# Optimization experiments

Hardware: AMD Instinct MI355X
Metric: run time of the kernel (lower is better)

Reference implementation:

```python
import jax, jax.numpy as jnp
import numpy as np


def setup_inputs() -> dict:
    key = jax.random.key(0)
    ks = jax.random.split(key, 4)
    B, C, H, W = 4, 512, 64, 64
    A = 512  # attention_dim
    x = jax.random.normal(ks[0], (B, C, H, W), dtype=jnp.float32)
    # 1x1 conv weights as [out_ch, in_ch] matrices (kaiming-like scale)
    scale = np.sqrt(2.0 / C).astype(np.float32)
    Wq = jax.random.normal(ks[1], (A, C), dtype=jnp.float32) * scale
    Wk = jax.random.normal(ks[2], (A, C), dtype=jnp.float32) * scale
    Wv = jax.random.normal(ks[3], (C, C), dtype=jnp.float32) * scale
    bq = jnp.zeros((A,), dtype=jnp.float32)
    bk = jnp.zeros((A,), dtype=jnp.float32)
    bv = jnp.zeros((C,), dtype=jnp.float32)
    return {"x": x, "Wq": Wq, "bq": bq, "Wk": Wk, "bk": bk, "Wv": Wv, "bv": bv}


def reference(x, Wq, bq, Wk, bk, Wv, bv):
    B, C, H, W = x.shape
    N = H * W
    xf = x.reshape(B, C, N)  # [B, C, N]
    # 1x1 convs == per-pixel channel matmuls
    q = jnp.einsum('ac,bcn->bna', Wq, xf) + bq[None, None, :]   # [B, N, A] (query, permuted)
    k = jnp.einsum('ac,bcn->ban', Wk, xf) + bk[None, :, None]   # [B, A, N] (key)
    v = jnp.einsum('oc,bcn->bno', Wv, xf) + bv[None, None, :]   # [B, N, C] (value, permuted)
    attn = jnp.einsum('bna,bam->bnm', q, k)                     # [B, N, N]
    attn = jax.nn.softmax(attn, axis=-2)                        # softmax over dim=-2 (queries)
    out = jnp.einsum('bnm,bmc->bnc', attn, v)                   # [B, N, C]
    # Faithful to torch: .view(B, C, H, W) reinterprets the [B, N, C] buffer
    out = out.reshape(B, C, H, W)
    return x + 0.1 * out
```

## Files before the change

kernel.cpp:

```cpp
#include <hip/hip_runtime.h>
#include <stdint.h>


#define LDT 40
#define SUB 5120

typedef _Float16 f16x8 __attribute__((ext_vector_type(8)));
typedef float f32x4 __attribute__((ext_vector_type(4)));

__device__ __forceinline__ void async16(const _Float16* g, _Float16* l)
{
  __builtin_amdgcn_global_load_lds(
      (const __attribute__((address_space(1))) void*)g,
      (__attribute__((address_space(3))) void*)l, 16, 0, 0);
}

#define WAIT_VM8() asm volatile("s_waitcnt vmcnt(8)" ::: "memory")
#define WAIT_VM0() asm volatile("s_waitcnt vmcnt(0)" ::: "memory")

template <int ASRC, int EPI, int NSUB, int STG>
__global__ void __launch_bounds__(256, 2) gemm_f16(
    const _Float16* __restrict__ Ap, long lda, long zsa,
    const _Float16* __restrict__ Bp, long ldb, long zsb,
    int kslice,
    const _Float16* __restrict__ fs16, long zsl,
    float* __restrict__ outF, _Float16* __restrict__ outH, long ldc, long zso,
    const float* __restrict__ bias0, const float* __restrict__ bias1,
    const float* __restrict__ xadd,
    float* __restrict__ pmax, float* __restrict__ psum, long zsp,
    float alpha)
{
  constexpr int SMEM_E = (STG == 1) ? (4 * NSUB * 4096) : (2 * NSUB * SUB);
  __shared__ _Float16 smem[SMEM_E];

  const int z = blockIdx.z;
  const long i0 = (long)blockIdx.x * 128;
  const long j0 = (long)blockIdx.y * 128;
  const int t = (int)threadIdx.x;
  const int lane = t & 63;
  const int wv = t >> 6;
  const int quad = lane >> 4;
  const int lrow = lane & 15;
  const int wm = (wv & 1) << 6;
  const int wn = (wv >> 1) << 6;

  f32x4 acc[4][4];
  const f32x4 fz = {0.f, 0.f, 0.f, 0.f};
#pragma unroll
  for (int a = 0; a < 4; a++)
#pragma unroll
    for (int b = 0; b < 4; b++) acc[a][b] = fz;

  if constexpr (STG == 0) {
    const int r0 = t >> 2;
    const int s0 = (t & 3) << 3;

    const _Float16* gA0 = Ap + z * zsa + (i0 + r0) * lda + s0;
    const _Float16* gA1 = gA0 + 64 * lda;
    const _Float16* gB0 = Bp + z * zsb + (j0 + r0) * ldb + s0;
    const _Float16* gB1 = gB0 + 64 * ldb;
    const int la0 = r0 * LDT + s0;
    const int la1 = (r0 + 64) * LDT + s0;

    for (int kk = 0; kk < kslice; kk += 32 * NSUB) {
      f16x8 va[NSUB][2], vb[NSUB][2];
#pragma unroll
      for (int s = 0; s < NSUB; s++) {
        va[s][0] = *(const f16x8*)(gA0 + kk + 32 * s);
        va[s][1] = *(const f16x8*)(gA1 + kk + 32 * s);
        vb[s][0] = *(const f16x8*)(gB0 + kk + 32 * s);
        vb[s][1] = *(const f16x8*)(gB1 + kk + 32 * s);
      }
      __syncthreads();
#pragma unroll
      for (int s = 0; s < NSUB; s++) {
        *(f16x8*)&smem[s * SUB + la0] = va[s][0];
        *(f16x8*)&smem[s * SUB + la1] = va[s][1];
        *(f16x8*)&smem[(NSUB + s) * SUB + la0] = vb[s][0];
        *(f16x8*)&smem[(NSUB + s) * SUB + la1] = vb[s][1];
      }
      __syncthreads();

#pragma unroll
      for (int h = 0; h < NSUB; h++) {
        const _Float16* pA = smem + h * SUB;
        const _Float16* pB = smem + (NSUB + h) * SUB;
        f16x8 fa[4], fb[4];
#pragma unroll
        for (int f = 0; f < 4; f++) {
          fa[f] = *(const f16x8*)&pA[(wm + f * 16 + lrow) * LDT + quad * 8];
          fb[f] = *(const f16x8*)&pB[(wn + f * 16 + lrow) * LDT + quad * 8];
        }
#pragma unroll
        for (int fm = 0; fm < 4; fm++)
#pragma unroll
          for (int fn = 0; fn < 4; fn++)
            acc[fm][fn] = __builtin_amdgcn_mfma_f32_16x16x32_f16(fa[fm], fb[fn], acc[fm][fn], 0, 0, 0);
      }
    }
  } else {
    constexpr int KSTEP = 32 * NSUB;
    constexpr int BUFE = 2 * NSUB * 4096;
    const int crow = lane >> 2;
    const int ks8 = (((lane & 3) ^ ((lane >> 3) & 3)) << 3);

    const _Float16* gAc0 = Ap + z * zsa + (i0 + 16 * wv + crow) * lda + ks8;
    const _Float16* gAc1 = gAc0 + 64 * lda;
    const _Float16* gBc0 = Bp + z * zsb + (j0 + 16 * wv + crow) * ldb + ks8;
    const _Float16* gBc1 = gBc0 + 64 * ldb;
    _Float16* ldsC0 = smem + wv * 512;
    _Float16* ldsC1 = smem + (wv + 4) * 512;

    const _Float16* fsZq = nullptr;
    if constexpr (ASRC == 1)
      fsZq = fs16 + z * zsl + (long)blockIdx.x * 4096 + quad * 8;

    const int qs = ((quad ^ ((lrow >> 1) & 3)) << 3);

    auto stage = [&](int buf, int kk) {
#pragma unroll
      for (int s = 0; s < NSUB; s++) {
        const int ab = buf * BUFE + s * 4096;
        const int bb = buf * BUFE + (NSUB + s) * 4096;
        async16(gAc0 + kk + 32 * s, ldsC0 + ab);
        async16(gAc1 + kk + 32 * s, ldsC1 + ab);
        async16(gBc0 + kk + 32 * s, ldsC0 + bb);
        async16(gBc1 + kk + 32 * s, ldsC1 + bb);
      }
    };

    stage(0, 0);
    int cur = 0;
    for (int kk = 0; kk < kslice; kk += KSTEP) {
      f16x8 fsv[NSUB];
      if constexpr (ASRC == 1) {
#pragma unroll
        for (int h = 0; h < NSUB; h++)
          fsv[h] = *(const f16x8*)(fsZq + kk + 32 * h);
      }
      if (kk + KSTEP < kslice) {
        stage(cur ^ 1, kk + KSTEP);
        WAIT_VM8();
      } else {
        WAIT_VM0();
      }
      __builtin_amdgcn_s_barrier();

#pragma unroll
      for (int h = 0; h < NSUB; h++) {
        const _Float16* pA = smem + cur * BUFE + h * 4096;
        const _Float16* pB = smem + cur * BUFE + (NSUB + h) * 4096;
        f16x8 fa[4], fb[4];
#pragma unroll
        for (int f = 0; f < 4; f++) {
          fa[f] = *(const f16x8*)&pA[(wm + f * 16 + lrow) * 32 + qs];
          fb[f] = *(const f16x8*)&pB[(wn + f * 16 + lrow) * 32 + qs];
        }
        if constexpr (ASRC == 1) {
#pragma unroll
          for (int f = 0; f < 4; f++) fa[f] = fa[f] * fsv[h];
        }
#pragma unroll
        for (int fm = 0; fm < 4; fm++)
#pragma unroll
          for (int fn = 0; fn < 4; fn++)
            acc[fm][fn] = __builtin_amdgcn_mfma_f32_16x16x32_f16(fa[fm], fb[fn], acc[fm][fn], 0, 0, 0);
      }
      __builtin_amdgcn_s_barrier();
      cur ^= 1;
    }
  }

  const long obase = (long)z * zso;

  if constexpr (EPI == 1 || EPI == 2) {
#pragma unroll
    for (int fm = 0; fm < 4; fm++) {
      const long gi0 = i0 + wm + fm * 16 + quad * 4;
#pragma unroll
      for (int fn = 0; fn < 4; fn++) {
        const long gj = j0 + wn + fn * 16 + lrow;
        float badd = 0.f;
        if constexpr (EPI == 1) badd = (gj < 512) ? bias0[gj] : bias1[gj - 512];
#pragma unroll
        for (int r = 0; r < 4; r++) {
          float v = acc[fm][fn][r];
          if constexpr (EPI == 1) v += badd;
          else v += bias0[gi0 + r];
          outH[obase + (gi0 + r) * ldc + gj] = (_Float16)v;
        }
      }
    }
  } else if constexpr (EPI == 3) {
#pragma unroll
    for (int fm = 0; fm < 4; fm++) {
      const long gi0 = i0 + wm + fm * 16 + quad * 4;
#pragma unroll
      for (int fn = 0; fn < 4; fn++) {
        const long gj = j0 + wn + fn * 16 + lrow;
#pragma unroll
        for (int r = 0; r < 4; r++) {
          const long o = obase + (gi0 + r) * ldc + gj;
          outF[o] = fmaf(alpha, acc[fm][fn][r], xadd[o]);
        }
      }
    }
  } else {
    __syncthreads();
    float* Ls = (float*)smem;
#pragma unroll
    for (int fn = 0; fn < 4; fn++) {
      float mx = -3.4e38f;
#pragma unroll
      for (int fm = 0; fm < 4; fm++)
#pragma unroll
        for (int r = 0; r < 4; r++) mx = fmaxf(mx, acc[fm][fn][r]);
      Ls[(wv * 4 + quad) * 64 + fn * 16 + lrow] = mx;
    }
    __syncthreads();
    {
      const int c = t & 127;
      const int h = t >> 7;
      const int wvv = ((c >> 6) << 1) + h;
      const int wc = c & 63;
      float M = -3.4e38f;
#pragma unroll
      for (int q = 0; q < 4; q++) M = fmaxf(M, Ls[(wvv * 4 + q) * 64 + wc]);
      Ls[1024 + h * 128 + c] = M;
    }
    __syncthreads();
    if (t < 128) {
      float Mcol = fmaxf(Ls[1024 + t], Ls[1152 + t]);
      pmax[z * zsp + (long)blockIdx.x * 4096 + j0 + t] = Mcol;
      Ls[1280 + t] = Mcol;
    }
    __syncthreads();
#pragma unroll
    for (int fn = 0; fn < 4; fn++) {
      const int colc = wn + fn * 16 + lrow;
      const float Mcol = Ls[1280 + colc];
      const long gj = j0 + colc;
      float sm = 0.f;
#pragma unroll
      for (int fm = 0; fm < 4; fm++) {
        const long gi0 = i0 + wm + fm * 16 + quad * 4;
#pragma unroll
        for (int r = 0; r < 4; r++) {
          float e = __expf(acc[fm][fn][r] - Mcol);
          sm += e;
          outH[obase + (gi0 + r) * ldc + gj] = (_Float16)e;
        }
      }
      Ls[(wv * 4 + quad) * 64 + fn * 16 + lrow] = sm;
    }
    __syncthreads();
    if (t < 128) {
      const int wc = t & 63;
      const int ch = t >> 6;
      float s = 0.f;
#pragma unroll
      for (int h = 0; h < 2; h++) {
        const int wvv = (ch << 1) + h;
#pragma unroll
        for (int q = 0; q < 4; q++) s += Ls[(wvv * 4 + q) * 64 + wc];
      }
      psum[z * zsp + (long)blockIdx.x * 4096 + j0 + t] = s;
    }
  }
}

__global__ void convert_weights(const float* __restrict__ Wq, const float* __restrict__ Wk,
                                const float* __restrict__ Wv,
                                _Float16* __restrict__ WQK, _Float16* __restrict__ Wv16)
{
  int idx = blockIdx.x * 256 + threadIdx.x;
  if (idx < 524288)
    WQK[idx] = (_Float16)((idx < 262144) ? Wq[idx] : Wk[idx - 262144]);
  else
    Wv16[idx - 524288] = (_Float16)Wv[idx - 524288];
}

__global__ void transpose_x(const float* __restrict__ x, _Float16* __restrict__ xT)
{
  __shared__ float tile[32][33];
  const int b = blockIdx.z;
  const int n0 = blockIdx.x * 32;
  const int c0 = blockIdx.y * 32;
  const int tx = threadIdx.x;
  const int ty = threadIdx.y;
  const float* xb = x + (long)b * 2097152;
#pragma unroll
  for (int k = 0; k < 4; k++)
    tile[ty + k * 8][tx] = xb[(long)(c0 + ty + k * 8) * 4096 + n0 + tx];
  __syncthreads();
  _Float16* xTb = xT + (long)b * 2097152;
#pragma unroll
  for (int k = 0; k < 4; k++)
    xTb[(long)(n0 + ty + k * 8) * 512 + c0 + tx] = (_Float16)tile[tx][ty + k * 8];
}

__global__ void stats_scale(const float* __restrict__ pmax, const float* __restrict__ psum,
                            _Float16* __restrict__ fs16)
{
  const int idx = blockIdx.x * 256 + threadIdx.x;
  const int z = idx >> 12;
  const int m = idx & 4095;
  const float* pm = pmax + (long)z * 131072 + m;
  const float* ps = psum + (long)z * 131072 + m;
  float M = -3.4e38f, S = 0.f;
  for (int i = 0; i < 32; i++) {
    float m2 = pm[(long)i * 4096], s2 = ps[(long)i * 4096];
    float nm = fmaxf(M, m2);
    S = S * __expf(M - nm) + s2 * __expf(m2 - nm);
    M = nm;
  }
  const float lse = M + __logf(S);
  _Float16* fo = fs16 + (long)z * 131072 + m;
  for (int i = 0; i < 32; i++)
    fo[(long)i * 4096] = (_Float16)__expf(pm[(long)i * 4096] - lse);
}

extern "C" void kernel_launch(void* const* d_in, const int* in_sizes, int n_in,
                              void* d_out, int out_size, void* d_ws, size_t ws_size,
                              hipStream_t stream)
{
  const float* x  = (const float*)d_in[0];
  const float* Wq = (const float*)d_in[1];
  const float* bq = (const float*)d_in[2];
  const float* Wk = (const float*)d_in[3];
  const float* bk = (const float*)d_in[4];
  const float* Wv = (const float*)d_in[5];
  const float* bv = (const float*)d_in[6];
  float* out = (float*)d_out;

  char* w = (char*)d_ws;
  _Float16* WQK   = (_Float16*)(w + 0);
  _Float16* Wv16  = (_Float16*)(w + 1048576);
  _Float16* xT    = (_Float16*)(w + 1572864);
  _Float16* QK    = (_Float16*)(w + 18350080);
  _Float16* Vt    = (_Float16*)(w + 51904512);
  float*    pmaxB = (float*)   (w + 68747264);
  float*    psumB = (float*)   (w + 70844416);
  _Float16* fs16  = (_Float16*)(w + 72941568);
  _Float16* S16   = (_Float16*)(w + 75038720);

  convert_weights<<<3072, 256, 0, stream>>>(Wq, Wk, Wv, WQK, Wv16);
  transpose_x<<<dim3(128, 16, 4), dim3(32, 8), 0, stream>>>(x, xT);

  gemm_f16<0, 1, 2, 0><<<dim3(32, 8, 4), 256, 0, stream>>>(
      xT, 512, 2097152L, WQK, 512, 0L, 512, nullptr, 0L,
      nullptr, QK, 1024, 4194304L, bq, bk, nullptr, nullptr, nullptr, 0L, 0.f);
  gemm_f16<0, 2, 2, 0><<<dim3(4, 32, 4), 256, 0, stream>>>(
      Wv16, 512, 0L, xT, 512, 2097152L, 512, nullptr, 0L,
      nullptr, Vt, 4096, 2097152L, bv, nullptr, nullptr, nullptr, nullptr, 0L, 0.f);
  gemm_f16<0, 4, 2, 1><<<dim3(32, 32, 4), 256, 0, stream>>>(
      QK, 1024, 4194304L, QK + 512, 1024, 4194304L, 512, nullptr, 0L,
      nullptr, S16, 4096, 16777216L, nullptr, nullptr, nullptr,
      pmaxB, psumB, 131072L, 0.f);
  stats_scale<<<64, 256, 0, stream>>>(pmaxB, psumB, fs16);
  gemm_f16<1, 3, 2, 1><<<dim3(32, 4, 4), 256, 0, stream>>>(
      S16, 4096, 16777216L, Vt, 4096, 2097152L, 4096, fs16, 131072L,
      out, nullptr, 512, 2097152L, nullptr, nullptr, x, nullptr, nullptr, 0L, 0.1f);
}
```

Before: 310.9 us.

## Restructure async GEMM pipeline into per-32-K ring buffers with tunable occupancy

The STG=1 GEMM path now stages one 32-wide K slice per buffer. The S·Q^T GEMM uses a double buffer with half the LDS, and launch bounds allow 4 blocks per CU. The attn·V GEMM uses a 4-deep ring that keeps 3 slices in flight. The per-column softmax scale vector is preloaded into LDS once instead of being read from global memory every iteration. This aims to raise occupancy and hide global-load latency, at the cost of more barriers per K unit and tighter register limits at occupancy 4.

```diff
diff --git a/kernel.cpp b/kernel.cpp
--- a/kernel.cpp
+++ b/kernel.cpp
@@ -15,11 +15,10 @@
       (__attribute__((address_space(3))) void*)l, 16, 0, 0);
 }
 
-#define WAIT_VM8() asm volatile("s_waitcnt vmcnt(8)" ::: "memory")
-#define WAIT_VM0() asm volatile("s_waitcnt vmcnt(0)" ::: "memory")
-
-template <int ASRC, int EPI, int NSUB, int STG>
-__global__ void __launch_bounds__(256, 2) gemm_f16(
+#define WVM(N) asm volatile("s_waitcnt vmcnt(" #N ")" ::: "memory")
+
+template <int ASRC, int EPI, int NSUB, int STG, int OCC>
+__global__ void __launch_bounds__(256, OCC) gemm_f16(
     const _Float16* __restrict__ Ap, long lda, long zsa,
     const _Float16* __restrict__ Bp, long ldb, long zsb,
     int kslice,
@@ -30,7 +29,8 @@
     float* __restrict__ pmax, float* __restrict__ psum, long zsp,
     float alpha)
 {
-  constexpr int SMEM_E = (STG == 1) ? (4 * NSUB * 4096) : (2 * NSUB * SUB);
+  constexpr int SMEM_E = (STG == 1) ? (NSUB * 8192 + (ASRC == 1 ? 4096 : 0))
+                                    : (2 * NSUB * SUB);
   __shared__ _Float16 smem[SMEM_E];
 
   const int z = blockIdx.z;
@@ -99,8 +99,6 @@
       }
     }
   } else {
-    constexpr int KSTEP = 32 * NSUB;
-    constexpr int BUFE = 2 * NSUB * 4096;
     const int crow = lane >> 2;
     const int ks8 = (((lane & 3) ^ ((lane >> 3) & 3)) << 3);
 
@@ -108,66 +106,65 @@
     const _Float16* gAc1 = gAc0 + 64 * lda;
     const _Float16* gBc0 = Bp + z * zsb + (j0 + 16 * wv + crow) * ldb + ks8;
     const _Float16* gBc1 = gBc0 + 64 * ldb;
-    _Float16* ldsC0 = smem + wv * 512;
-    _Float16* ldsC1 = smem + (wv + 4) * 512;
-
-    const _Float16* fsZq = nullptr;
+
+    const int qs = ((quad ^ ((lrow >> 1) & 3)) << 3);
+
+    auto stage = [&](int buf, int kk2) {
+      _Float16* base = smem + buf * 8192;
+      async16(gAc0 + kk2, base + wv * 512);
+      async16(gAc1 + kk2, base + 2048 + wv * 512);
+      async16(gBc0 + kk2, base + 4096 + wv * 512);
+      async16(gBc1 + kk2, base + 6144 + wv * 512);
+    };
+
+    _Float16* fsL = nullptr;
+    if constexpr (ASRC == 1) {
+      fsL = smem + NSUB * 8192;
+      const _Float16* fsrc = fs16 + z * zsl + (long)blockIdx.x * 4096;
+      *(f16x8*)&fsL[t * 16] = *(const f16x8*)&fsrc[t * 16];
+      *(f16x8*)&fsL[t * 16 + 8] = *(const f16x8*)&fsrc[t * 16 + 8];
+    }
+    stage(0, 0);
+    if constexpr (NSUB == 4) { stage(1, 32); stage(2, 64); }
     if constexpr (ASRC == 1)
-      fsZq = fs16 + z * zsl + (long)blockIdx.x * 4096 + quad * 8;
-
-    const int qs = ((quad ^ ((lrow >> 1) & 3)) << 3);
-
-    auto stage = [&](int buf, int kk) {
-#pragma unroll
-      for (int s = 0; s < NSUB; s++) {
-        const int ab = buf * BUFE + s * 4096;
-        const int bb = buf * BUFE + (NSUB + s) * 4096;
-        async16(gAc0 + kk + 32 * s, ldsC0 + ab);
-        async16(gAc1 + kk + 32 * s, ldsC1 + ab);
-        async16(gBc0 + kk + 32 * s, ldsC0 + bb);
-        async16(gBc1 + kk + 32 * s, ldsC1 + bb);
-      }
-    };
-
-    stage(0, 0);
-    int cur = 0;
-    for (int kk = 0; kk < kslice; kk += KSTEP) {
-      f16x8 fsv[NSUB];
+      asm volatile("s_waitcnt lgkmcnt(0)" ::: "memory");
+    __builtin_amdgcn_s_barrier();
+
+    int ib = 0;
+    for (int kk = 0; kk < kslice; kk += 32, ++ib) {
+      const int rem = kslice - kk;
+      if constexpr (NSUB == 4) {
+        if (rem > 96) { stage((ib + 3) & 3, kk + 96); WVM(12); }
+        else if (rem > 64) { WVM(8); }
+        else if (rem > 32) { WVM(4); }
+        else { WVM(0); }
+      } else {
+        if (rem > 32) { stage((ib + 1) & 1, kk + 32); WVM(4); }
+        else { WVM(0); }
+      }
+      __builtin_amdgcn_s_barrier();
+
+      const int cur = ib & (NSUB - 1);
+      const _Float16* pA = smem + cur * 8192;
+      const _Float16* pB = pA + 4096;
+      f16x8 fa[4], fb[4];
+#pragma unroll
+      for (int f = 0; f < 4; f++) {
+        fa[f] = *(const f16x8*)&pA[(wm + f * 16 + lrow) * 32 + qs];
+        fb[f] = *(const f16x8*)&pB[(wn + f * 16 + lrow) * 32 + qs];
+      }
       if constexpr (ASRC == 1) {
-#pragma unroll
-        for (int h = 0; h < NSUB; h++)
-          fsv[h] = *(const f16x8*)(fsZq + kk + 32 * h);
-      }
-      if (kk + KSTEP < kslice) {
-        stage(cur ^ 1, kk + KSTEP);
-        WAIT_VM8();
-      } else {
-        WAIT_VM0();
-      }
+        const f16x8 fsv = *(const f16x8*)&fsL[kk + quad * 8];
+#pragma unroll
+        for (int f = 0; f < 4; f++) fa[f] = fa[f] * fsv;
+      }
+#pragma unroll
+      for (int fm = 0; fm < 4; fm++)
+#pragma unroll
+        for (int fn = 0; fn < 4; fn++)
+          acc[fm][fn] = __builtin_amdgcn_mfma_f32_16x16x32_f16(fa[fm], fb[fn], acc[fm][fn], 0, 0, 0);
+
       __builtin_amdgcn_s_barrier();
-
-#pragma unroll
-      for (int h = 0; h < NSUB; h++) {
-        const _Float16* pA = smem + cur * BUFE + h * 4096;
-        const _Float16* pB = smem + cur * BUFE + (NSUB + h) * 4096;
-        f16x8 fa[4], fb[4];
-#pragma unroll
-        for (int f = 0; f < 4; f++) {
-          fa[f] = *(const f16x8*)&pA[(wm + f * 16 + lrow) * 32 + qs];
-          fb[f] = *(const f16x8*)&pB[(wn + f * 16 + lrow) * 32 + qs];
-        }
-        if constexpr (ASRC == 1) {
-#pragma unroll
-          for (int f = 0; f < 4; f++) fa[f] = fa[f] * fsv[h];
-        }
-#pragma unroll
-        for (int fm = 0; fm < 4; fm++)
-#pragma unroll
-          for (int fn = 0; fn < 4; fn++)
-            acc[fm][fn] = __builtin_amdgcn_mfma_f32_16x16x32_f16(fa[fm], fb[fn], acc[fm][fn], 0, 0, 0);
-      }
-      __builtin_amdgcn_s_barrier();
-      cur ^= 1;
     }
   }
 
@@ -347,18 +344,18 @@
   convert_weights<<<3072, 256, 0, stream>>>(Wq, Wk, Wv, WQK, Wv16);
   transpose_x<<<dim3(128, 16, 4), dim3(32, 8), 0, stream>>>(x, xT);
 
-  gemm_f16<0, 1, 2, 0><<<dim3(32, 8, 4), 256, 0, stream>>>(
+  gemm_f16<0, 1, 2, 0, 2><<<dim3(32, 8, 4), 256, 0, stream>>>(
       xT, 512, 2097152L, WQK, 512, 0L, 512, nullptr, 0L,
       nullptr, QK, 1024, 4194304L, bq, bk, nullptr, nullptr, nullptr, 0L, 0.f);
-  gemm_f16<0, 2, 2, 0><<<dim3(4, 32, 4), 256, 0, stream>>>(
+  gemm_f16<0, 2, 2, 0, 2><<<dim3(4, 32, 4), 256, 0, stream>>>(
       Wv16, 512, 0L, xT, 512, 2097152L, 512, nullptr, 0L,
       nullptr, Vt, 4096, 2097152L, bv, nullptr, nullptr, nullptr, nullptr, 0L, 0.f);
-  gemm_f16<0, 4, 2, 1><<<dim3(32, 32, 4), 256, 0, stream>>>(
+  gemm_f16<0, 4, 2, 1, 4><<<dim3(32, 32, 4), 256, 0, stream>>>(
       QK, 1024, 4194304L, QK + 512, 1024, 4194304L, 512, nullptr, 0L,
       nullptr, S16, 4096, 16777216L, nullptr, nullptr, nullptr,
       pmaxB, psumB, 131072L, 0.f);
   stats_scale<<<64, 256, 0, stream>>>(pmaxB, psumB, fs16);
-  gemm_f16<1, 3, 2, 1><<<dim3(32, 4, 4), 256, 0, stream>>>(
+  gemm_f16<1, 3, 4, 1, 2><<<dim3(32, 4, 4), 256, 0, stream>>>(
       S16, 4096, 16777216L, Vt, 4096, 2097152L, 4096, fs16, 131072L,
       out, nullptr, 512, 2097152L, nullptr, nullptr, x, nullptr, nullptr, 0L, 0.1f);
 }
```

After: 319.9 us. 2.9% more time.

## Add dedicated 256x256-tile scores kernel with interleaved async staging and MFMA priority

Applied to the files above, without the earlier changes.

Replaces the generic 128x128 QK^T score GEMM with a specialized 512-thread kernel that computes 256x256 tiles. Each k-step is split into four phases that interleave async global-to-LDS loads with MFMA bursts, and s_setprio raises wave priority during the MFMA bursts. The larger tile roughly halves per-tile Q/K reloads and halves the number of partial column max/sum records. stats_scale and the final PV GEMM's scale indexing are adjusted to match, using 16 row partials and blockIdx.x>>1. The 128KB LDS footprint and the large accumulator array limit occupancy, which may reduce latency hiding.

```diff
diff --git a/kernel.cpp b/kernel.cpp
--- a/kernel.cpp
+++ b/kernel.cpp
@@ -15,22 +15,193 @@
       (__attribute__((address_space(3))) void*)l, 16, 0, 0);
 }
 
-#define WAIT_VM8() asm volatile("s_waitcnt vmcnt(8)" ::: "memory")
-#define WAIT_VM0() asm volatile("s_waitcnt vmcnt(0)" ::: "memory")
-
-template <int ASRC, int EPI, int NSUB, int STG>
-__global__ void __launch_bounds__(256, 2) gemm_f16(
+#define WVM(N) asm volatile("s_waitcnt vmcnt(" #N ")" ::: "memory")
+
+__global__ void __launch_bounds__(512, 2) scores256(
+    const _Float16* __restrict__ QKp, _Float16* __restrict__ S16,
+    float* __restrict__ pmax, float* __restrict__ psum)
+{
+  __shared__ _Float16 smem[65536];
+
+  const int z = blockIdx.z;
+  const long i0 = (long)blockIdx.x * 256;
+  const long j0 = (long)blockIdx.y * 256;
+  const int t = (int)threadIdx.x;
+  const int lane = t & 63;
+  const int wv = t >> 6;
+  const int quad = lane >> 4;
+  const int lrow = lane & 15;
+  const int wr = wv >> 2;
+  const int wc = wv & 3;
+  const int wm = wr << 7;
+  const int wn = wc << 6;
+
+  const _Float16* Qz = QKp + (long)z * 4194304;
+  const _Float16* Kz = QKp + 512 + (long)z * 4194304;
+
+  const int crow = lane >> 2;
+  const int ks8 = (((lane & 3) ^ ((lane >> 3) & 3)) << 3);
+  const _Float16* gQ = Qz + (i0 + wv * 16 + crow) * 1024 + ks8;
+  const _Float16* gK = Kz + (j0 + wv * 16 + crow) * 1024 + ks8;
+
+  auto stage = [&](int buf, int kt2, int isB, int kh) {
+    const _Float16* src = isB ? gK : gQ;
+    const long col = (long)kt2 * 64 + kh * 32;
+    _Float16* d = smem + buf * 32768 + isB * 16384 + kh * 4096 + wv * 512;
+    async16(src + col, d);
+    async16(src + col + 128 * 1024, d + 8192);
+  };
+
+  const int qs = ((quad ^ ((lrow >> 1) & 3)) << 3);
+
+  f32x4 acc[8][4];
+  const f32x4 fz = {0.f, 0.f, 0.f, 0.f};
+#pragma unroll
+  for (int a = 0; a < 8; a++)
+#pragma unroll
+    for (int b = 0; b < 4; b++) acc[a][b] = fz;
+
+  stage(0, 0, 1, 0); stage(0, 0, 0, 0); stage(0, 0, 1, 1); stage(0, 0, 0, 1);
+  stage(1, 1, 1, 0); stage(1, 1, 0, 0); stage(1, 1, 1, 1);
+  WVM(6);
+  __builtin_amdgcn_s_barrier();
+
+  for (int kt = 0; kt < 8; ++kt) {
+    const int buf = kt & 1;
+    const _Float16* pA = smem + buf * 32768 + wr * 8192;
+    const _Float16* pB = smem + buf * 32768 + 16384 + (wc >> 1) * 8192 + (wc & 1) * 2048;
+    f16x8 fa[4], fb[4];
+
+#pragma unroll
+    for (int f = 0; f < 4; f++) {
+      fa[f] = *(const f16x8*)&pA[(f * 16 + lrow) * 32 + qs];
+      fb[f] = *(const f16x8*)&pB[(f * 16 + lrow) * 32 + qs];
+    }
+    if (kt + 1 < 8) stage(buf ^ 1, kt + 1, 0, 1);
+    __builtin_amdgcn_s_barrier();
+    __builtin_amdgcn_sched_barrier(0);
+    __builtin_amdgcn_s_setprio(1);
+#pragma unroll
+    for (int fm = 0; fm < 4; fm++)
+#pragma unroll
+      for (int fn = 0; fn < 4; fn++)
+        acc[fm][fn] = __builtin_amdgcn_mfma_f32_16x16x32_f16(fa[fm], fb[fn], acc[fm][fn], 0, 0, 0);
+    __builtin_amdgcn_s_setprio(0);
+    __builtin_amdgcn_sched_barrier(0);
+    __builtin_amdgcn_s_barrier();
+
+#pragma unroll
+    for (int f = 0; f < 4; f++)
+      fa[f] = *(const f16x8*)&pA[((f + 4) * 16 + lrow) * 32 + qs];
+    if (kt + 2 < 8) stage(buf, kt + 2, 1, 0);
+    __builtin_amdgcn_s_barrier();
+    __builtin_amdgcn_sched_barrier(0);
+    __builtin_amdgcn_s_setprio(1);
+#pragma unroll
+    for (int fm = 0; fm < 4; fm++)
+#pragma unroll
+      for (int fn = 0; fn < 4; fn++)
+        acc[4 + fm][fn] = __builtin_amdgcn_mfma_f32_16x16x32_f16(fa[fm], fb[fn], acc[4 + fm][fn], 0, 0, 0);
+    __builtin_amdgcn_s_setprio(0);
+    __builtin_amdgcn_sched_barrier(0);
+    __builtin_amdgcn_s_barrier();
+
+#pragma unroll
+    for (int f = 0; f < 4; f++) {
+      fa[f] = *(const f16x8*)&pA[4096 + (f * 16 + lrow) * 32 + qs];
+      fb[f] = *(const f16x8*)&pB[4096 + (f * 16 + lrow) * 32 + qs];
+    }
+    if (kt + 2 < 8) stage(buf, kt + 2, 0, 0);
+    __builtin_amdgcn_s_barrier();
+    __builtin_amdgcn_sched_barrier(0);
+    __builtin_amdgcn_s_setprio(1);
+#pragma unroll
+    for (int fm = 0; fm < 4; fm++)
+#pragma unroll
+      for (int fn = 0; fn < 4; fn++)
+        acc[fm][fn] = __builtin_amdgcn_mfma_f32_16x16x32_f16(fa[fm], fb[fn], acc[fm][fn], 0, 0, 0);
+    __builtin_amdgcn_s_setprio(0);
+    __builtin_amdgcn_sched_barrier(0);
+    __builtin_amdgcn_s_barrier();
+
+#pragma unroll
+    for (int f = 0; f < 4; f++)
+      fa[f] = *(const f16x8*)&pA[4096 + ((f + 4) * 16 + lrow) * 32 + qs];
+    if (kt + 2 < 8) stage(buf, kt + 2, 1, 1);
+    if (kt + 2 < 8) { WVM(6); }
+    else if (kt + 1 < 8) { WVM(0); }
+    __builtin_amdgcn_s_barrier();
+    __builtin_amdgcn_sched_barrier(0);
+    __builtin_amdgcn_s_setprio(1);
+#pragma unroll
+    for (int fm = 0; fm < 4; fm++)
+#pragma unroll
+      for (int fn = 0; fn < 4; fn++)
+        acc[4 + fm][fn] = __builtin_amdgcn_mfma_f32_16x16x32_f16(fa[fm], fb[fn], acc[4 + fm][fn], 0, 0, 0);
+    __builtin_amdgcn_s_setprio(0);
+    __builtin_amdgcn_sched_barrier(0);
+    __builtin_amdgcn_s_barrier();
+  }
+
+  __syncthreads();
+  float* Ls = (float*)smem;
+  const long obase = (long)z * 16777216;
+#pragma unroll
+  for (int fn = 0; fn < 4; fn++) {
+    float mx = -3.4e38f;
+#pragma unroll
+    for (int fm = 0; fm < 8; fm++)
+#pragma unroll
+      for (int r = 0; r < 4; r++) mx = fmaxf(mx, acc[fm][fn][r]);
+    Ls[(wr * 4 + quad) * 256 + wn + fn * 16 + lrow] = mx;
+  }
+  __syncthreads();
+  if (t < 256) {
+    float M = -3.4e38f;
+#pragma unroll
+    for (int p = 0; p < 8; p++) M = fmaxf(M, Ls[p * 256 + t]);
+    pmax[(long)z * 65536 + (long)blockIdx.x * 4096 + j0 + t] = M;
+    Ls[2048 + t] = M;
+  }
+  __syncthreads();
+#pragma unroll
+  for (int fn = 0; fn < 4; fn++) {
+    const int colc = wn + fn * 16 + lrow;
+    const float Mcol = Ls[2048 + colc];
+    const long gj = j0 + colc;
+    float sm = 0.f;
+#pragma unroll
+    for (int fm = 0; fm < 8; fm++) {
+      const long gi0 = i0 + wm + fm * 16 + quad * 4;
+#pragma unroll
+      for (int r = 0; r < 4; r++) {
+        float e = __expf(acc[fm][fn][r] - Mcol);
+        sm += e;
+        S16[obase + (gi0 + r) * 4096 + gj] = (_Float16)e;
+      }
+    }
+    Ls[(wr * 4 + quad) * 256 + colc] = sm;
+  }
+  __syncthreads();
+  if (t < 256) {
+    float s = 0.f;
+#pragma unroll
+    for (int p = 0; p < 8; p++) s += Ls[p * 256 + t];
+    psum[(long)z * 65536 + (long)blockIdx.x * 4096 + j0 + t] = s;
+  }
+}
+
+template <int ASRC, int EPI, int NSUB, int STG, int OCC>
+__global__ void __launch_bounds__(256, OCC) gemm_f16(
     const _Float16* __restrict__ Ap, long lda, long zsa,
     const _Float16* __restrict__ Bp, long ldb, long zsb,
     int kslice,
     const _Float16* __restrict__ fs16, long zsl,
     float* __restrict__ outF, _Float16* __restrict__ outH, long ldc, long zso,
     const float* __restrict__ bias0, const float* __restrict__ bias1,
-    const float* __restrict__ xadd,
-    float* __restrict__ pmax, float* __restrict__ psum, long zsp,
-    float alpha)
-{
-  constexpr int SMEM_E = (STG == 1) ? (4 * NSUB * 4096) : (2 * NSUB * SUB);
+    const float* __restrict__ xadd, float alpha)
+{
+  constexpr int SMEM_E = (STG == 2) ? (4 * NSUB * 4096) : (2 * NSUB * SUB);
   __shared__ _Float16 smem[SMEM_E];
 
   const int z = blockIdx.z;
@@ -113,7 +284,7 @@
 
     const _Float16* fsZq = nullptr;
     if constexpr (ASRC == 1)
-      fsZq = fs16 + z * zsl + (long)blockIdx.x * 4096 + quad * 8;
+      fsZq = fs16 + z * zsl + (long)(blockIdx.x >> 1) * 4096 + quad * 8;
 
     const int qs = ((quad ^ ((lrow >> 1) & 3)) << 3);
 
@@ -140,9 +311,9 @@
       }
       if (kk + KSTEP < kslice) {
         stage(cur ^ 1, kk + KSTEP);
-        WAIT_VM8();
+        WVM(8);
       } else {
-        WAIT_VM0();
+        WVM(0);
       }
       __builtin_amdgcn_s_barrier();
 
@@ -191,7 +362,7 @@
         }
       }
     }
-  } else if constexpr (EPI == 3) {
+  } else {
 #pragma unroll
     for (int fm = 0; fm < 4; fm++) {
       const long gi0 = i0 + wm + fm * 16 + quad * 4;
@@ -204,67 +375,6 @@
           outF[o] = fmaf(alpha, acc[fm][fn][r], xadd[o]);
         }
       }
-    }
-  } else {
-    __syncthreads();
-    float* Ls = (float*)smem;
-#pragma unroll
-    for (int fn = 0; fn < 4; fn++) {
-      float mx = -3.4e38f;
-#pragma unroll
-      for (int fm = 0; fm < 4; fm++)
-#pragma unroll
-        for (int r = 0; r < 4; r++) mx = fmaxf(mx, acc[fm][fn][r]);
-      Ls[(wv * 4 + quad) * 64 + fn * 16 + lrow] = mx;
-    }
-    __syncthreads();
-    {
-      const int c = t & 127;
-      const int h = t >> 7;
-      const int wvv = ((c >> 6) << 1) + h;
-      const int wc = c & 63;
-      float M = -3.4e38f;
-#pragma unroll
-      for (int q = 0; q < 4; q++) M = fmaxf(M, Ls[(wvv * 4 + q) * 64 + wc]);
-      Ls[1024 + h * 128 + c] = M;
-    }
-    __syncthreads();
-    if (t < 128) {
-      float Mcol = fmaxf(Ls[1024 + t], Ls[1152 + t]);
-      pmax[z * zsp + (long)blockIdx.x * 4096 + j0 + t] = Mcol;
-      Ls[1280 + t] = Mcol;
-    }
-    __syncthreads();
-#pragma unroll
-    for (int fn = 0; fn < 4; fn++) {
-      const int colc = wn + fn * 16 + lrow;
-      const float Mcol = Ls[1280 + colc];
-      const long gj = j0 + colc;
-      float sm = 0.f;
-#pragma unroll
-      for (int fm = 0; fm < 4; fm++) {
-        const long gi0 = i0 + wm + fm * 16 + quad * 4;
-#pragma unroll
-        for (int r = 0; r < 4; r++) {
-          float e = __expf(acc[fm][fn][r] - Mcol);
-          sm += e;
-          outH[obase + (gi0 + r) * ldc + gj] = (_Float16)e;
-        }
-      }
-      Ls[(wv * 4 + quad) * 64 + fn * 16 + lrow] = sm;
-    }
-    __syncthreads();
-    if (t < 128) {
-      const int wc = t & 63;
-      const int ch = t >> 6;
-      float s = 0.f;
-#pragma unroll
-      for (int h = 0; h < 2; h++) {
-        const int wvv = (ch << 1) + h;
-#pragma unroll
-        for (int q = 0; q < 4; q++) s += Ls[(wvv * 4 + q) * 64 + wc];
-      }
-      psum[z * zsp + (long)blockIdx.x * 4096 + j0 + t] = s;
     }
   }
 }
@@ -305,18 +415,18 @@
   const int idx = blockIdx.x * 256 + threadIdx.x;
   const int z = idx >> 12;
   const int m = idx & 4095;
-  const float* pm = pmax + (long)z * 131072 + m;
-  const float* ps = psum + (long)z * 131072 + m;
+  const float* pm = pmax + (long)z * 65536 + m;
+  const float* ps = psum + (long)z * 65536 + m;
   float M = -3.4e38f, S = 0.f;
-  for (int i = 0; i < 32; i++) {
+  for (int i = 0; i < 16; i++) {
     float m2 = pm[(long)i * 4096], s2 = ps[(long)i * 4096];
     float nm = fmaxf(M, m2);
     S = S * __expf(M - nm) + s2 * __expf(m2 - nm);
     M = nm;
   }
   const float lse = M + __logf(S);
-  _Float16* fo = fs16 + (long)z * 131072 + m;
-  for (int i = 0; i < 32; i++)
+  _Float16* fo = fs16 + (long)z * 65536 + m;
+  for (int i = 0; i < 16; i++)
     fo[(long)i * 4096] = (_Float16)__expf(pm[(long)i * 4096] - lse);
 }
 
@@ -347,18 +457,15 @@
   convert_weights<<<3072, 256, 0, stream>>>(Wq, Wk, Wv, WQK, Wv16);
   transpose_x<<<dim3(128, 16, 4), dim3(32, 8), 0, stream>>>(x, xT);
 
-  gemm_f16<0, 1, 2, 0><<<dim3(32, 8, 4), 256, 0, stream>>>(
+  gemm_f16<0, 1, 2, 0, 2><<<dim3(32, 8, 4), 256, 0, stream>>>(
       xT, 512, 2097152L, WQK, 512, 0L, 512, nullptr, 0L,
-      nullptr, QK, 1024, 4194304L, bq, bk, nullptr, nullptr, nullptr, 0L, 0.f);
-  gemm_f16<0, 2, 2, 0><<<dim3(4, 32, 4), 256, 0, stream>>>(
+      nullptr, QK, 1024, 4194304L, bq, bk, nullptr, 0.f);
+  gemm_f16<0, 2, 2, 0, 2><<<dim3(4, 32, 4), 256, 0, stream>>>(
       Wv16, 512, 0L, xT, 512, 2097152L, 512, nullptr, 0L,
-      nullptr, Vt, 4096, 2097152L, bv, nullptr, nullptr, nullptr, nullptr, 0L, 0.f);
-  gemm_f16<0, 4, 2, 1><<<dim3(32, 32, 4), 256, 0, stream>>>(
-      QK, 1024, 4194304L, QK + 512, 1024, 4194304L, 512, nullptr, 0L,
-      nullptr, S16, 4096, 16777216L, nullptr, nullptr, nullptr,
-      pmaxB, psumB, 131072L, 0.f);
+      nullptr, Vt, 4096, 2097152L, bv, nullptr, nullptr, 0.f);
+  scores256<<<dim3(16, 16, 4), 512, 0, stream>>>(QK, S16, pmaxB, psumB);
   stats_scale<<<64, 256, 0, stream>>>(pmaxB, psumB, fs16);
-  gemm_f16<1, 3, 2, 1><<<dim3(32, 4, 4), 256, 0, stream>>>(
-      S16, 4096, 16777216L, Vt, 4096, 2097152L, 4096, fs16, 131072L,
-      out, nullptr, 512, 2097152L, nullptr, nullptr, x, nullptr, nullptr, 0L, 0.1f);
-}
+  gemm_f16<1, 3, 2, 2, 2><<<dim3(32, 4, 4), 256, 0, stream>>>(
+      S16, 4096, 16777216L, Vt, 4096, 2097152L, 4096, fs16, 65536L,
+      out, nullptr, 512, 2097152L, nullptr, nullptr, x, 0.1f);
+}
```

After: 336.9 us. 8.4% more time.
